# Kernel tuning notes

Hardware: AMD Instinct MI355X
Metric: run time of the kernel (lower is better)

Reference implementation:

```python
import jax, jax.numpy as jnp
import numpy as np

EPS = 1e-08


def setup_inputs() -> dict:
    key = jax.random.key(0)
    k1, k2 = jax.random.split(key)
    query_features = jax.random.normal(k1, (64, 1024, 32, 32), dtype=jnp.float32)
    support_features = jax.random.normal(k2, (25, 1024, 32, 32), dtype=jnp.float32)
    return {"query_features": query_features, "support_features": support_features}


def reference(query_features, support_features):
    B, C, h, w = support_features.shape
    NQ = query_features.shape[0]
    # Covariance over channels: flatten support to (C, B*h*w), center, GEMM.
    support = jnp.transpose(support_features, (1, 0, 2, 3)).reshape(C, -1)
    centered = support - jnp.mean(support, axis=1, keepdims=True)
    N = B * h * w
    cov = (centered @ centered.T) / (N - 1 + EPS)  # (C, C)
    # Queries: (NQ, C, d), L2-normalize each channel row over spatial dim.
    q = query_features.reshape(NQ, C, -1)
    q = q / (jnp.linalg.norm(q, axis=2, keepdims=True) + EPS)
    # diag(q^T cov q) without materializing (d, d): cov@q then elementwise reduce over C.
    cq = jnp.einsum('cD,nDd->ncd', cov, q)  # (NQ, C, d)
    scores = jnp.mean(jnp.sum(q * cq, axis=1), axis=1)  # (NQ,)
    return scores
```

## Files before the change

kernel.cpp:

```cpp
#include <hip/hip_runtime.h>

#define NQ   64
#define CCH  1024
#define DSP  1024
#define NSUP 25600
#define NKT  400

typedef __attribute__((ext_vector_type(4))) float f32x4;
typedef __attribute__((ext_vector_type(8))) __bf16 bf16x8;

#define WAITVM(N) asm volatile("s_waitcnt vmcnt(" #N ")" ::: "memory")
#define WAITLGKM0() asm volatile("s_waitcnt lgkmcnt(0)" ::: "memory")
#define BAR() __builtin_amdgcn_s_barrier()
#define SCHED0() __builtin_amdgcn_sched_barrier(0)

__device__ inline unsigned short f2bf(float x) {
  unsigned u = __builtin_bit_cast(unsigned, x);
  u += 0x7fffu + ((u >> 16) & 1u);
  return (unsigned short)(u >> 16);
}

__global__ __launch_bounds__(256) void zero_kernel(float4* __restrict__ cov4,
                                                   float4* __restrict__ out4) {
  const int i = blockIdx.x * 256 + threadIdx.x;
  cov4[i] = make_float4(0.f, 0.f, 0.f, 0.f);
  if (i < 16) out4[i] = make_float4(0.f, 0.f, 0.f, 0.f);
}


__global__ __launch_bounds__(512) void mean_center_kernel(
    const float* __restrict__ sup, float* __restrict__ mean,
    unsigned short* __restrict__ Sb, int write_sb) {
  __shared__ float4 row[6400];
  __shared__ float red[512];
  const int c = blockIdx.x;
  const int tid = threadIdx.x;
  float s = 0.f;
  for (int qd = tid; qd < 6400; qd += 512) {
    const int b = qd >> 8, s4 = (qd & 255) << 2;
    const float4 v = *(const float4*)(sup + ((size_t)b * CCH + c) * DSP + s4);
    row[qd] = v;
    s += v.x + v.y + v.z + v.w;
  }
  red[tid] = s;
  __syncthreads();
  for (int st = 256; st > 0; st >>= 1) {
    if (tid < st) red[tid] += red[tid + st];
    __syncthreads();
  }
  const float m = red[0] * (1.0f / 25600.0f);
  if (tid == 0) mean[c] = m;
  if (write_sb) {
    for (int qd = tid; qd < 6400; qd += 512) {
      const float4 v = row[qd];
      const int b = qd >> 8, s4 = (qd & 255) << 2;
      ushort4 o;
      o.x = f2bf(v.x - m); o.y = f2bf(v.y - m);
      o.z = f2bf(v.z - m); o.w = f2bf(v.w - m);
      *(ushort4*)(Sb + (size_t)c * NSUP + b * DSP + s4) = o;
    }
  }
}

__global__ __launch_bounds__(256) void qnorm_kernel(
    const float* __restrict__ q, float* __restrict__ qfac,
    unsigned short* __restrict__ Qb, int write_qb) {
  const int row = blockIdx.x * 4 + (threadIdx.x >> 6);
  const int l = threadIdx.x & 63;
  const float4* src = (const float4*)(q + (size_t)row * DSP);
  float4 v[4];
  float ss = 0.f;
#pragma unroll
  for (int i = 0; i < 4; ++i) {
    v[i] = src[l + 64 * i];
    ss += v[i].x * v[i].x + v[i].y * v[i].y + v[i].z * v[i].z + v[i].w * v[i].w;
  }
#pragma unroll
  for (int off = 32; off > 0; off >>= 1) ss += __shfl_xor(ss, off);
  const float f = 1.0f / (sqrtf(ss) + 1e-8f);
  if (l == 0) qfac[row] = f;
  if (write_qb) {
#pragma unroll
    for (int i = 0; i < 4; ++i) {
      ushort4 o;
      o.x = f2bf(v[i].x * f); o.y = f2bf(v[i].y * f);
      o.z = f2bf(v[i].z * f); o.w = f2bf(v[i].w * f);
      *(ushort4*)(Qb + (size_t)row * DSP + (size_t)(l + 64 * i) * 4) = o;
    }
  }
}


__device__ inline void rd4(const unsigned short* base, int r0, int col, int lr, bf16x8 f[4]) {
#pragma unroll
  for (int i = 0; i < 4; ++i)
    f[i] = *(const bf16x8*)(const void*)(base + (r0 + i * 16 + lr) * 64 + col);
}
__device__ inline void mfma16(const bf16x8 a[4], const bf16x8 b[4], f32x4 (*acc)[4]) {
  __builtin_amdgcn_s_setprio(1);
#pragma unroll
  for (int i = 0; i < 4; ++i)
#pragma unroll
    for (int j = 0; j < 4; ++j)
      acc[i][j] = __builtin_amdgcn_mfma_f32_16x16x32_bf16(a[i], b[j], acc[i][j], 0, 0, 0);
  __builtin_amdgcn_s_setprio(0);
}

__device__ inline void stage_glds(const unsigned short* __restrict__ src, int ld,
                                  int row0, int k0, unsigned short* lds) {
  const int tid = threadIdx.x;
  const int w = tid >> 6;
#pragma unroll
  for (int it = 0; it < 4; ++it) {
    const int ci = it * 256 + tid;
    const int r = ci >> 3;
    const int kc = ((ci & 7) ^ (r & 7)) << 3;
    const unsigned short* g = src + (size_t)(row0 + r) * ld + k0 + kc;
    unsigned short* lb = lds + ((it * 256 + w * 64) << 3);
    __builtin_amdgcn_global_load_lds((const __attribute__((address_space(1))) void*)g,
                                     (__attribute__((address_space(3))) void*)lb,
                                     16, 0, 0);
  }
}

__device__ inline void stage256g(const unsigned short* __restrict__ src, int ld,
                                 int row0, int k0, unsigned short* lds_base) {
  const int tid = threadIdx.x;
  const int wid = tid >> 6;
#pragma unroll
  for (int it = 0; it < 4; ++it) {
    const int ci = it * 512 + tid;
    const int r = ci >> 3;
    const int kc = ((ci & 7) ^ (r & 7)) << 3;
    const unsigned short* g = src + (size_t)(row0 + r) * ld + k0 + kc;
    unsigned short* lb = lds_base + ((it * 512 + (wid << 6)) << 3);
    __builtin_amdgcn_global_load_lds((const __attribute__((address_space(1))) void*)g,
                                     (__attribute__((address_space(3))) void*)lb,
                                     16, 0, 0);
  }
}

template <int NT>
__device__ inline void loop256(const unsigned short* __restrict__ src, int ld,
                               int rowA, int rowB, int k0, bool diag,
                               unsigned short* lds,
                               int wm, int wn, int lr, int kg, int sw,
                               f32x4 (*acc)[4]) {
  stage256g(src, ld, rowA, k0, lds);
  if (!diag) stage256g(src, ld, rowB, k0, lds + 16384);
  stage256g(src, ld, rowA, k0 + 64, lds + 32768);
  if (!diag) stage256g(src, ld, rowB, k0 + 64, lds + 32768 + 16384);

  for (int t = 0; t < NT; ++t) {
    const int cb = (t & 1) << 15;
    if (t < NT - 1) { if (diag) { WAITVM(4); } else { WAITVM(8); } }
    else { WAITVM(0); }
    BAR(); SCHED0();
    const unsigned short* A = lds + cb + wm * 8192;
    const unsigned short* B = lds + cb + (diag ? 0 : 16384) + (wn >> 1) * 8192;
    const int brow = (wn & 1) * 64;
    bf16x8 a[4], b[4];
    {
      const int col = kg ^ sw;
      rd4(B, brow, col, lr, b);
      rd4(A, 0, col, lr, a);
      mfma16(a, b, &acc[0]);
      rd4(A, 64, col, lr, a);
      mfma16(a, b, &acc[4]);
    }
    {
      const int col = (32 + kg) ^ sw;
      rd4(B, brow, col, lr, b);
      rd4(A, 0, col, lr, a);
      mfma16(a, b, &acc[0]);
      rd4(A, 64, col, lr, a);
      WAITLGKM0();
      BAR(); SCHED0();
      if (t + 2 < NT) {
        stage256g(src, ld, rowA, k0 + (t + 2) * 64, lds + cb);
        if (!diag) stage256g(src, ld, rowB, k0 + (t + 2) * 64, lds + cb + 16384);
      }
      mfma16(a, b, &acc[4]);
    }
  }
}

__device__ inline void decode_tile8(int t, int& ti, int& tj) {
  int rem = t; ti = 0;
  while (rem >= 8 - ti) { rem -= 8 - ti; ++ti; }
  tj = ti + rem;
}
__device__ inline void decode_pair4(int p, int& ti, int& tj) {
  int rem = p; ti = 0;
  while (rem >= 4 - ti) { rem -= 4 - ti; ++ti; }
  tj = ti + rem;
}

__global__ __launch_bounds__(256) void cov128_kernel(
    const unsigned short* __restrict__ Sb, float* __restrict__ cov) {
  __shared__ unsigned short clds[32768];
  const int wg = blockIdx.x;
  const int ks = wg % 7;
  int ti, tj; decode_tile8(wg / 7, ti, tj);
  const bool diag = (ti == tj);
  const int tid = threadIdx.x, l = tid & 63, w = tid >> 6;
  const int wr = (w >> 1) * 64, wc = (w & 1) * 64, lr = l & 15, kg = (l >> 4) * 8;
  const int sw = (lr & 7) << 3;
  f32x4 acc[4][4];
#pragma unroll
  for (int i = 0; i < 4; ++i)
#pragma unroll
    for (int j = 0; j < 4; ++j) acc[i][j] = 0.f;

  const int kt0 = (NKT * ks) / 7;
  const int nt = (NKT * (ks + 1)) / 7 - kt0;
  const int kbase = kt0 * 64;

  stage_glds(Sb, NSUP, ti * 128, kbase, clds);
  if (!diag) stage_glds(Sb, NSUP, tj * 128, kbase, clds + 8192);
  stage_glds(Sb, NSUP, ti * 128, kbase + 64, clds + 16384);
  if (!diag) stage_glds(Sb, NSUP, tj * 128, kbase + 64, clds + 16384 + 8192);
  for (int t = 0; t < nt; ++t) {
    const int cb = (t & 1) * 16384;
    if (t < nt - 1) { if (diag) { WAITVM(4); } else { WAITVM(8); } }
    else { WAITVM(0); }
    BAR(); SCHED0();
    const unsigned short* A = clds + cb;
    const unsigned short* B = diag ? A : A + 8192;
    const int col0 = kg ^ sw, col1 = (32 + kg) ^ sw;
    bf16x8 a[4], b[4];
    rd4(A, wr, col0, lr, a);
    rd4(B, wc, col0, lr, b);
    mfma16(a, b, (f32x4(*)[4])acc);
    rd4(A, wr, col1, lr, a);
    rd4(B, wc, col1, lr, b);
    WAITLGKM0();
    BAR(); SCHED0();
    if (t + 2 < nt) {
      const int k2 = kbase + (t + 2) * 64;
      stage_glds(Sb, NSUP, ti * 128, k2, clds + cb);
      if (!diag) stage_glds(Sb, NSUP, tj * 128, k2, clds + cb + 8192);
    }
    mfma16(a, b, (f32x4(*)[4])acc);
  }

  const float scale = 1.0f / (25599.0f + 1e-8f);
  const int rbase = ti * 128 + wr + (l >> 4) * 4;
  const int cbase = tj * 128 + wc + (l & 15);
#pragma unroll
  for (int i = 0; i < 4; ++i)
#pragma unroll
    for (int j = 0; j < 4; ++j)
#pragma unroll
      for (int r = 0; r < 4; ++r)
        atomicAdd(&cov[(size_t)(rbase + i * 16 + r) * CCH + cbase + j * 16],
                  acc[i][j][r] * scale);
}

__global__ __launch_bounds__(512, 2) void gram256_kernel(
    const unsigned short* __restrict__ Qb, const float* __restrict__ cov,
    float* __restrict__ out) {
  __shared__ unsigned short lds[65536];
  const int wg = blockIdx.x;
  const int xcd = wg & 7, slot = wg >> 3;
  const int n = xcd * 8 + slot / 10;
  int ti, tj; decode_pair4(slot % 10, ti, tj);
  const bool diag = (ti == tj);
  const int tid = threadIdx.x, l = tid & 63, wid = tid >> 6;
  const int wm = wid >> 2, wn = wid & 3;
  const int lr = l & 15, kg = (l >> 4) * 8;
  const int sw = (lr & 7) << 3;
  const unsigned short* Qn = Qb + (size_t)n * CCH * DSP;

  f32x4 acc[8][4];
#pragma unroll
  for (int i = 0; i < 8; ++i)
#pragma unroll
    for (int j = 0; j < 4; ++j) acc[i][j] = 0.f;

  loop256<16>(Qn, DSP, ti * 256, tj * 256, 0, diag, lds,
              wm, wn, lr, kg, sw, acc);

  float wgt;
  if (!diag) wgt = 2.0f;
  else if (wm == 0 && (wn >> 1) == 1) wgt = 2.0f;
  else if (wm == 1 && (wn >> 1) == 0) wgt = 0.0f;
  else wgt = 1.0f;

  float s = 0.f;
  if (wgt != 0.0f) {
    const int rbase = ti * 256 + wm * 128 + (l >> 4) * 4;
    const int cbase = tj * 256 + wn * 64 + (l & 15);
#pragma unroll
    for (int i = 0; i < 8; ++i)
#pragma unroll
      for (int j = 0; j < 4; ++j)
#pragma unroll
        for (int r = 0; r < 4; ++r)
          s += acc[i][j][r] * cov[(size_t)(rbase + i * 16 + r) * CCH + cbase + j * 16];
  }
  s *= wgt * (1.0f / 1024.0f);
#pragma unroll
  for (int off = 32; off > 0; off >>= 1) s += __shfl_xor(s, off);
  if (l == 0) atomicAdd(&out[n], s);
}

__device__ inline void mfma16s(const bf16x8 a[4], const bf16x8 b[4], f32x4 acc[4][4]) {
#pragma unroll
  for (int i = 0; i < 4; ++i)
#pragma unroll
    for (int j = 0; j < 4; ++j)
      acc[i][j] = __builtin_amdgcn_mfma_f32_16x16x32_bf16(a[i], b[j], acc[i][j], 0, 0, 0);
}

__device__ inline void stage_sup_f32(const float* __restrict__ sup,
                                     const float* __restrict__ mean,
                                     int row0, int k0, unsigned short* lds) {
  const int tid = threadIdx.x;
#pragma unroll
  for (int it = 0; it < 4; ++it) {
    const int ci = it * 256 + tid;
    const int r = ci >> 3, kc = (ci & 7) << 3;
    const int c = row0 + r;
    const int k = k0 + kc;
    const int b = k >> 10, sp = k & 1023;
    const float4* gp = (const float4*)(sup + ((size_t)b * CCH + c) * DSP + sp);
    const float4 v0 = gp[0], v1 = gp[1];
    const float m = mean[c];
    union { unsigned short h[8]; int4 q; } pk;
    pk.h[0] = f2bf(v0.x - m); pk.h[1] = f2bf(v0.y - m);
    pk.h[2] = f2bf(v0.z - m); pk.h[3] = f2bf(v0.w - m);
    pk.h[4] = f2bf(v1.x - m); pk.h[5] = f2bf(v1.y - m);
    pk.h[6] = f2bf(v1.z - m); pk.h[7] = f2bf(v1.w - m);
    *(int4*)(lds + (size_t)(r * 8 + ((ci & 7) ^ (r & 7))) * 8) = pk.q;
  }
}
__device__ inline void stage_q_f32(const float* __restrict__ qn,
                                   const float* __restrict__ qfacn,
                                   int row0, int k0, unsigned short* lds) {
  const int tid = threadIdx.x;
#pragma unroll
  for (int it = 0; it < 4; ++it) {
    const int ci = it * 256 + tid;
    const int r = ci >> 3, kc = (ci & 7) << 3;
    const int c = row0 + r;
    const float4* gp = (const float4*)(qn + (size_t)c * DSP + k0 + kc);
    const float4 v0 = gp[0], v1 = gp[1];
    const float f = qfacn[c];
    union { unsigned short h[8]; int4 q; } pk;
    pk.h[0] = f2bf(v0.x * f); pk.h[1] = f2bf(v0.y * f);
    pk.h[2] = f2bf(v0.z * f); pk.h[3] = f2bf(v0.w * f);
    pk.h[4] = f2bf(v1.x * f); pk.h[5] = f2bf(v1.y * f);
    pk.h[6] = f2bf(v1.z * f); pk.h[7] = f2bf(v1.w * f);
    *(int4*)(lds + (size_t)(r * 8 + ((ci & 7) ^ (r & 7))) * 8) = pk.q;
  }
}
__device__ inline void compute_step(const unsigned short* lA, const unsigned short* lB,
                                    int wr, int wc, int lr, int kg, f32x4 acc[4][4]) {
  const int sc = (lr & 7) << 3;
#pragma unroll
  for (int kk = 0; kk < 64; kk += 32) {
    const int col = (kk + kg) ^ sc;
    bf16x8 a[4], b[4];
    rd4(lA, wr, col, lr, a);
    rd4(lB, wc, col, lr, b);
    mfma16s(a, b, acc);
  }
}

__global__ __launch_bounds__(256) void cov_kernel_f32(
    const float* __restrict__ sup, const float* __restrict__ mean,
    float* __restrict__ cov) {
  __shared__ unsigned short clds[32768];
  const int wg = blockIdx.x;
  const int ks = wg & 7;
  int ti, tj; decode_tile8(wg >> 3, ti, tj);
  const bool diag = (ti == tj);
  const int tid = threadIdx.x, l = tid & 63, w = tid >> 6;
  const int wr = (w >> 1) * 64, wc = (w & 1) * 64, lr = l & 15, kg = (l >> 4) * 8;
  f32x4 acc[4][4];
#pragma unroll
  for (int i = 0; i < 4; ++i)
#pragma unroll
    for (int j = 0; j < 4; ++j) acc[i][j] = 0.f;

  const int kbase = ks * (NSUP / 8);
  stage_sup_f32(sup, mean, ti * 128, kbase, clds);
  if (!diag) stage_sup_f32(sup, mean, tj * 128, kbase, clds + 8192);
  __syncthreads();
  for (int kt = 0; kt < 50; ++kt) {
    const int cb = (kt & 1) * 16384;
    const int nb = cb ^ 16384;
    if (kt + 1 < 50) {
      const int k1 = kbase + (kt + 1) * 64;
      stage_sup_f32(sup, mean, ti * 128, k1, clds + nb);
      if (!diag) stage_sup_f32(sup, mean, tj * 128, k1, clds + nb + 8192);
    }
    compute_step(clds + cb, diag ? clds + cb : clds + cb + 8192, wr, wc, lr, kg, acc);
    __syncthreads();
  }
  const float scale = 1.0f / (25599.0f + 1e-8f);
  const int rbase = ti * 128 + wr + (l >> 4) * 4;
  const int cbase = tj * 128 + wc + (l & 15);
#pragma unroll
  for (int i = 0; i < 4; ++i)
#pragma unroll
    for (int j = 0; j < 4; ++j)
#pragma unroll
      for (int r = 0; r < 4; ++r)
        atomicAdd(&cov[(size_t)(rbase + i * 16 + r) * CCH + cbase + j * 16],
                  acc[i][j][r] * scale);
}

__global__ __launch_bounds__(256) void gram_kernel_f32(
    const float* __restrict__ q, const float* __restrict__ qfac,
    const float* __restrict__ cov, float* __restrict__ out) {
  __shared__ unsigned short lA[2][128 * 64];
  __shared__ unsigned short lB[2][128 * 64];
  const int wg = blockIdx.x;
  const int xcd = wg & 7, slot = wg >> 3;
  const int n = xcd * 8 + slot / 36;
  int ti, tj; decode_tile8(slot % 36, ti, tj);
  const bool diag = (ti == tj);
  const int tid = threadIdx.x, l = tid & 63, w = tid >> 6;
  const int wr = (w >> 1) * 64, wc = (w & 1) * 64, lr = l & 15, kg = (l >> 4) * 8;
  f32x4 acc[4][4];
#pragma unroll
  for (int i = 0; i < 4; ++i)
#pragma unroll
    for (int j = 0; j < 4; ++j) acc[i][j] = 0.f;

  const float* qn = q + (size_t)n * CCH * DSP;
  const float* qfacn = qfac + (size_t)n * CCH;

  stage_q_f32(qn, qfacn, ti * 128, 0, lA[0]);
  if (!diag) stage_q_f32(qn, qfacn, tj * 128, 0, lB[0]);
  __syncthreads();
  int cur = 0;
  for (int kt = 0; kt < 16; ++kt) {
    if (kt + 1 < 16) {
      const int k1 = (kt + 1) * 64;
      stage_q_f32(qn, qfacn, ti * 128, k1, lA[cur ^ 1]);
      if (!diag) stage_q_f32(qn, qfacn, tj * 128, k1, lB[cur ^ 1]);
    }
    compute_step(lA[cur], diag ? lA[cur] : lB[cur], wr, wc, lr, kg, acc);
    __syncthreads();
    cur ^= 1;
  }

  float s = 0.f;
  const int rbase = ti * 128 + wr + (l >> 4) * 4;
  const int cbase = tj * 128 + wc + (l & 15);
#pragma unroll
  for (int i = 0; i < 4; ++i)
#pragma unroll
    for (int j = 0; j < 4; ++j)
#pragma unroll
      for (int r = 0; r < 4; ++r)
        s += acc[i][j][r] * cov[(size_t)(rbase + i * 16 + r) * CCH + cbase + j * 16];
  if (!diag) s *= 2.0f;
  s *= (1.0f / 1024.0f);
#pragma unroll
  for (int off = 32; off > 0; off >>= 1) s += __shfl_xor(s, off);
  if (l == 0) atomicAdd(&out[n], s);
}

extern "C" void kernel_launch(void* const* d_in, const int* in_sizes, int n_in,
                              void* d_out, int out_size, void* d_ws, size_t ws_size,
                              hipStream_t stream) {
  const float* q = (const float*)d_in[0];
  const float* sup = (const float*)d_in[1];
  float* out = (float*)d_out;

  char* ws = (char*)d_ws;
  float* mean = (float*)ws;
  float* qfac = (float*)(ws + (4 << 10));
  float* cov  = (float*)(ws + (4 << 10) + (256 << 10));
  unsigned short* Sb = (unsigned short*)(ws + (4 << 10) + (256 << 10) + (4 << 20));
  unsigned short* Qb = Sb + (size_t)CCH * NSUP;
  const size_t need_fat = (size_t)(4 << 10) + (256 << 10) + (4 << 20) +
                          (size_t)CCH * NSUP * 2 + (size_t)NQ * CCH * DSP * 2;
  const bool fat = ws_size >= need_fat;

  zero_kernel<<<1024, 256, 0, stream>>>((float4*)cov, (float4*)out);

  mean_center_kernel<<<CCH, 512, 0, stream>>>(sup, mean, Sb, fat ? 1 : 0);
  qnorm_kernel<<<NQ * CCH / 4, 256, 0, stream>>>(q, qfac, Qb, fat ? 1 : 0);

  if (fat) {
    cov128_kernel<<<dim3(252), 256, 0, stream>>>(Sb, cov);
    gram256_kernel<<<dim3(640), 512, 0, stream>>>(Qb, cov, out);
  } else {
    cov_kernel_f32<<<dim3(288), 256, 0, stream>>>(sup, mean, cov);
    gram_kernel_f32<<<dim3(8 * 8 * 36), 256, 0, stream>>>(q, qfac, cov, out);
  }
}
```

Before: 271.5 us.

## Fuse covariance and gram kernels into one persistent launch with atomic ticket ordering

Merges the cov128 and gram256 kernels into a single 640-block launch. Blocks take a ticket from an atomic counter, and the first 252 tickets first compute a covariance split-K tile (now 512 threads, with the k-halves split across waves) and then signal a completion counter. Every block then computes its query gram tile and spin-waits on that counter only before its final cov-weighted reduction. This overlaps the gram MFMA work with the covariance phase and removes a kernel boundary. In exchange it adds spin-wait and atomic traffic, and the cov blocks occupy 512-thread slots with a different wave split.

```diff
diff --git a/kernel.cpp b/kernel.cpp
--- a/kernel.cpp
+++ b/kernel.cpp
@@ -5,6 +5,7 @@
 #define DSP  1024
 #define NSUP 25600
 #define NKT  400
+#define NCOV 252
 
 typedef __attribute__((ext_vector_type(4))) float f32x4;
 typedef __attribute__((ext_vector_type(8))) __bf16 bf16x8;
@@ -21,10 +22,12 @@
 }
 
 __global__ __launch_bounds__(256) void zero_kernel(float4* __restrict__ cov4,
-                                                   float4* __restrict__ out4) {
+                                                   float4* __restrict__ out4,
+                                                   int* __restrict__ ctrs) {
   const int i = blockIdx.x * 256 + threadIdx.x;
   cov4[i] = make_float4(0.f, 0.f, 0.f, 0.f);
   if (i < 16) out4[i] = make_float4(0.f, 0.f, 0.f, 0.f);
+  if (blockIdx.x == 0 && threadIdx.x < 64) ctrs[threadIdx.x] = 0;
 }
 
 
@@ -106,17 +109,17 @@
   __builtin_amdgcn_s_setprio(0);
 }
 
-__device__ inline void stage_glds(const unsigned short* __restrict__ src, int ld,
-                                  int row0, int k0, unsigned short* lds) {
+__device__ inline void stage128_512(const unsigned short* __restrict__ src, int ld,
+                                    int row0, int k0, unsigned short* lds) {
   const int tid = threadIdx.x;
   const int w = tid >> 6;
 #pragma unroll
-  for (int it = 0; it < 4; ++it) {
-    const int ci = it * 256 + tid;
+  for (int it = 0; it < 2; ++it) {
+    const int ci = it * 512 + tid;
     const int r = ci >> 3;
     const int kc = ((ci & 7) ^ (r & 7)) << 3;
     const unsigned short* g = src + (size_t)(row0 + r) * ld + k0 + kc;
-    unsigned short* lb = lds + ((it * 256 + w * 64) << 3);
+    unsigned short* lb = lds + ((it * 512 + (w << 6)) << 3);
     __builtin_amdgcn_global_load_lds((const __attribute__((address_space(1))) void*)g,
                                      (__attribute__((address_space(3))) void*)lb,
                                      16, 0, 0);
@@ -140,20 +143,108 @@
   }
 }
 
-template <int NT>
-__device__ inline void loop256(const unsigned short* __restrict__ src, int ld,
-                               int rowA, int rowB, int k0, bool diag,
-                               unsigned short* lds,
-                               int wm, int wn, int lr, int kg, int sw,
-                               f32x4 (*acc)[4]) {
-  stage256g(src, ld, rowA, k0, lds);
-  if (!diag) stage256g(src, ld, rowB, k0, lds + 16384);
-  stage256g(src, ld, rowA, k0 + 64, lds + 32768);
-  if (!diag) stage256g(src, ld, rowB, k0 + 64, lds + 32768 + 16384);
-
-  for (int t = 0; t < NT; ++t) {
-    const int cb = (t & 1) << 15;
-    if (t < NT - 1) { if (diag) { WAITVM(4); } else { WAITVM(8); } }
+__device__ inline void decode_tile8(int t, int& ti, int& tj) {
+  int rem = t; ti = 0;
+  while (rem >= 8 - ti) { rem -= 8 - ti; ++ti; }
+  tj = ti + rem;
+}
+__device__ inline void decode_pair4(int p, int& ti, int& tj) {
+  int rem = p; ti = 0;
+  while (rem >= 4 - ti) { rem -= 4 - ti; ++ti; }
+  tj = ti + rem;
+}
+
+__global__ __launch_bounds__(512, 2) void fused_kernel(
+    const unsigned short* __restrict__ Sb, const unsigned short* __restrict__ Qb,
+    float* __restrict__ cov, int* __restrict__ ctrs, float* __restrict__ out) {
+  __shared__ unsigned short lds[65536];
+  __shared__ int tick_s;
+  const int tid = threadIdx.x, l = tid & 63, wid = tid >> 6;
+  if (tid == 0) tick_s = atomicAdd(&ctrs[0], 1);
+  __syncthreads();
+  const int t = tick_s;
+  const int lr = l & 15, kg = (l >> 4) * 8;
+  const int sw = (lr & 7) << 3;
+
+  if (t < NCOV) {
+    const int ks = t % 7;
+    int ci_, cj_; decode_tile8(t / 7, ci_, cj_);
+    const bool cdiag = (ci_ == cj_);
+    const int quad = wid & 3, kh = wid >> 2;
+    const int wr = (quad >> 1) * 64, wc = (quad & 1) * 64;
+    const int kt0 = (NKT * ks) / 7;
+    const int nt = (NKT * (ks + 1)) / 7 - kt0;
+    const int kbase = kt0 * 64;
+    f32x4 acc4[4][4];
+#pragma unroll
+    for (int i = 0; i < 4; ++i)
+#pragma unroll
+      for (int j = 0; j < 4; ++j) acc4[i][j] = 0.f;
+
+    stage128_512(Sb, NSUP, ci_ * 128, kbase, lds);
+    if (!cdiag) stage128_512(Sb, NSUP, cj_ * 128, kbase, lds + 8192);
+    stage128_512(Sb, NSUP, ci_ * 128, kbase + 64, lds + 16384);
+    if (!cdiag) stage128_512(Sb, NSUP, cj_ * 128, kbase + 64, lds + 16384 + 8192);
+    for (int k = 0; k < nt; ++k) {
+      const int cb = (k & 1) * 16384;
+      if (k < nt - 1) { if (cdiag) { WAITVM(2); } else { WAITVM(4); } }
+      else { WAITVM(0); }
+      BAR(); SCHED0();
+      const unsigned short* A = lds + cb;
+      const unsigned short* B = cdiag ? A : A + 8192;
+      const int col = (kh * 32 + kg) ^ sw;
+      bf16x8 a[4], b[4];
+      rd4(A, wr, col, lr, a);
+      rd4(B, wc, col, lr, b);
+      WAITLGKM0();
+      BAR(); SCHED0();
+      if (k + 2 < nt) {
+        const int k2 = kbase + (k + 2) * 64;
+        stage128_512(Sb, NSUP, ci_ * 128, k2, lds + cb);
+        if (!cdiag) stage128_512(Sb, NSUP, cj_ * 128, k2, lds + cb + 8192);
+      }
+      mfma16(a, b, acc4);
+    }
+    const float scale = 1.0f / (25599.0f + 1e-8f);
+    const int rbase = ci_ * 128 + wr + (l >> 4) * 4;
+    const int cbase = cj_ * 128 + wc + (l & 15);
+#pragma unroll
+    for (int i = 0; i < 4; ++i)
+#pragma unroll
+      for (int j = 0; j < 4; ++j)
+#pragma unroll
+        for (int r = 0; r < 4; ++r)
+          atomicAdd(&cov[(size_t)(rbase + i * 16 + r) * CCH + cbase + j * 16],
+                    acc4[i][j][r] * scale);
+    __threadfence();
+    __syncthreads();
+    if (tid == 0)
+      __hip_atomic_fetch_add(&ctrs[1], 1, __ATOMIC_RELEASE, __HIP_MEMORY_SCOPE_AGENT);
+    __syncthreads();
+  }
+
+  const int xcd = t & 7, slot = t >> 3;
+  const int n = xcd * 8 + slot / 10;
+  int ti, tj; decode_pair4(slot % 10, ti, tj);
+  const bool diag = (ti == tj);
+  const int wm = wid >> 2, wn = wid & 3;
+  const unsigned short* Qn = Qb + (size_t)n * CCH * DSP;
+  const int rowA = ti * 256, rowB = tj * 256;
+
+  f32x4 acc[8][4];
+#pragma unroll
+  for (int i = 0; i < 8; ++i)
+#pragma unroll
+    for (int j = 0; j < 4; ++j) acc[i][j] = 0.f;
+
+  stage256g(Qn, DSP, rowA, 0, lds);
+  if (!diag) stage256g(Qn, DSP, rowB, 0, lds + 16384);
+  stage256g(Qn, DSP, rowA, 64, lds + 32768);
+  if (!diag) stage256g(Qn, DSP, rowB, 64, lds + 32768 + 16384);
+
+  for (int k = 0; k < 16; ++k) {
+    const int cb = (k & 1) << 15;
+    if (k < 15) { if (diag) { WAITVM(4); } else { WAITVM(8); } }
     else { WAITVM(0); }
     BAR(); SCHED0();
     const unsigned short* A = lds + cb + wm * 8192;
@@ -176,110 +267,19 @@
       rd4(A, 64, col, lr, a);
       WAITLGKM0();
       BAR(); SCHED0();
-      if (t + 2 < NT) {
-        stage256g(src, ld, rowA, k0 + (t + 2) * 64, lds + cb);
-        if (!diag) stage256g(src, ld, rowB, k0 + (t + 2) * 64, lds + cb + 16384);
+      if (k + 2 < 16) {
+        stage256g(Qn, DSP, rowA, (k + 2) * 64, lds + cb);
+        if (!diag) stage256g(Qn, DSP, rowB, (k + 2) * 64, lds + cb + 16384);
       }
       mfma16(a, b, &acc[4]);
     }
   }
-}
-
-__device__ inline void decode_tile8(int t, int& ti, int& tj) {
-  int rem = t; ti = 0;
-  while (rem >= 8 - ti) { rem -= 8 - ti; ++ti; }
-  tj = ti + rem;
-}
-__device__ inline void decode_pair4(int p, int& ti, int& tj) {
-  int rem = p; ti = 0;
-  while (rem >= 4 - ti) { rem -= 4 - ti; ++ti; }
-  tj = ti + rem;
-}
-
-__global__ __launch_bounds__(256) void cov128_kernel(
-    const unsigned short* __restrict__ Sb, float* __restrict__ cov) {
-  __shared__ unsigned short clds[32768];
-  const int wg = blockIdx.x;
-  const int ks = wg % 7;
-  int ti, tj; decode_tile8(wg / 7, ti, tj);
-  const bool diag = (ti == tj);
-  const int tid = threadIdx.x, l = tid & 63, w = tid >> 6;
-  const int wr = (w >> 1) * 64, wc = (w & 1) * 64, lr = l & 15, kg = (l >> 4) * 8;
-  const int sw = (lr & 7) << 3;
-  f32x4 acc[4][4];
-#pragma unroll
-  for (int i = 0; i < 4; ++i)
-#pragma unroll
-    for (int j = 0; j < 4; ++j) acc[i][j] = 0.f;
-
-  const int kt0 = (NKT * ks) / 7;
-  const int nt = (NKT * (ks + 1)) / 7 - kt0;
-  const int kbase = kt0 * 64;
-
-  stage_glds(Sb, NSUP, ti * 128, kbase, clds);
-  if (!diag) stage_glds(Sb, NSUP, tj * 128, kbase, clds + 8192);
-  stage_glds(Sb, NSUP, ti * 128, kbase + 64, clds + 16384);
-  if (!diag) stage_glds(Sb, NSUP, tj * 128, kbase + 64, clds + 16384 + 8192);
-  for (int t = 0; t < nt; ++t) {
-    const int cb = (t & 1) * 16384;
-    if (t < nt - 1) { if (diag) { WAITVM(4); } else { WAITVM(8); } }
-    else { WAITVM(0); }
-    BAR(); SCHED0();
-    const unsigned short* A = clds + cb;
-    const unsigned short* B = diag ? A : A + 8192;
-    const int col0 = kg ^ sw, col1 = (32 + kg) ^ sw;
-    bf16x8 a[4], b[4];
-    rd4(A, wr, col0, lr, a);
-    rd4(B, wc, col0, lr, b);
-    mfma16(a, b, (f32x4(*)[4])acc);
-    rd4(A, wr, col1, lr, a);
-    rd4(B, wc, col1, lr, b);
-    WAITLGKM0();
-    BAR(); SCHED0();
-    if (t + 2 < nt) {
-      const int k2 = kbase + (t + 2) * 64;
-      stage_glds(Sb, NSUP, ti * 128, k2, clds + cb);
-      if (!diag) stage_glds(Sb, NSUP, tj * 128, k2, clds + cb + 8192);
-    }
-    mfma16(a, b, (f32x4(*)[4])acc);
-  }
-
-  const float scale = 1.0f / (25599.0f + 1e-8f);
-  const int rbase = ti * 128 + wr + (l >> 4) * 4;
-  const int cbase = tj * 128 + wc + (l & 15);
-#pragma unroll
-  for (int i = 0; i < 4; ++i)
-#pragma unroll
-    for (int j = 0; j < 4; ++j)
-#pragma unroll
-      for (int r = 0; r < 4; ++r)
-        atomicAdd(&cov[(size_t)(rbase + i * 16 + r) * CCH + cbase + j * 16],
-                  acc[i][j][r] * scale);
-}
-
-__global__ __launch_bounds__(512, 2) void gram256_kernel(
-    const unsigned short* __restrict__ Qb, const float* __restrict__ cov,
-    float* __restrict__ out) {
-  __shared__ unsigned short lds[65536];
-  const int wg = blockIdx.x;
-  const int xcd = wg & 7, slot = wg >> 3;
-  const int n = xcd * 8 + slot / 10;
-  int ti, tj; decode_pair4(slot % 10, ti, tj);
-  const bool diag = (ti == tj);
-  const int tid = threadIdx.x, l = tid & 63, wid = tid >> 6;
-  const int wm = wid >> 2, wn = wid & 3;
-  const int lr = l & 15, kg = (l >> 4) * 8;
-  const int sw = (lr & 7) << 3;
-  const unsigned short* Qn = Qb + (size_t)n * CCH * DSP;
-
-  f32x4 acc[8][4];
-#pragma unroll
-  for (int i = 0; i < 8; ++i)
-#pragma unroll
-    for (int j = 0; j < 4; ++j) acc[i][j] = 0.f;
-
-  loop256<16>(Qn, DSP, ti * 256, tj * 256, 0, diag, lds,
-              wm, wn, lr, kg, sw, acc);
+
+  if (tid == 0) {
+    while (__hip_atomic_load(&ctrs[1], __ATOMIC_ACQUIRE, __HIP_MEMORY_SCOPE_AGENT) < NCOV)
+      __builtin_amdgcn_s_sleep(8);
+  }
+  __syncthreads();
 
   float wgt;
   if (!diag) wgt = 2.0f;
@@ -296,8 +296,12 @@
 #pragma unroll
       for (int j = 0; j < 4; ++j)
 #pragma unroll
-        for (int r = 0; r < 4; ++r)
-          s += acc[i][j][r] * cov[(size_t)(rbase + i * 16 + r) * CCH + cbase + j * 16];
+        for (int r = 0; r < 4; ++r) {
+          const float cv = __hip_atomic_load(
+              &cov[(size_t)(rbase + i * 16 + r) * CCH + cbase + j * 16],
+              __ATOMIC_RELAXED, __HIP_MEMORY_SCOPE_AGENT);
+          s += acc[i][j][r] * cv;
+        }
   }
   s *= wgt * (1.0f / 1024.0f);
 #pragma unroll
@@ -476,20 +480,20 @@
   float* mean = (float*)ws;
   float* qfac = (float*)(ws + (4 << 10));
   float* cov  = (float*)(ws + (4 << 10) + (256 << 10));
-  unsigned short* Sb = (unsigned short*)(ws + (4 << 10) + (256 << 10) + (4 << 20));
+  int* ctrs = (int*)(ws + (4 << 10) + (256 << 10) + (4 << 20));
+  unsigned short* Sb = (unsigned short*)(ws + (4 << 10) + (256 << 10) + (4 << 20) + 256);
   unsigned short* Qb = Sb + (size_t)CCH * NSUP;
-  const size_t need_fat = (size_t)(4 << 10) + (256 << 10) + (4 << 20) +
+  const size_t need_fat = (size_t)(4 << 10) + (256 << 10) + (4 << 20) + 256 +
                           (size_t)CCH * NSUP * 2 + (size_t)NQ * CCH * DSP * 2;
   const bool fat = ws_size >= need_fat;
 
-  zero_kernel<<<1024, 256, 0, stream>>>((float4*)cov, (float4*)out);
+  zero_kernel<<<1024, 256, 0, stream>>>((float4*)cov, (float4*)out, ctrs);
 
   mean_center_kernel<<<CCH, 512, 0, stream>>>(sup, mean, Sb, fat ? 1 : 0);
   qnorm_kernel<<<NQ * CCH / 4, 256, 0, stream>>>(q, qfac, Qb, fat ? 1 : 0);
 
   if (fat) {
-    cov128_kernel<<<dim3(252), 256, 0, stream>>>(Sb, cov);
-    gram256_kernel<<<dim3(640), 512, 0, stream>>>(Qb, cov, out);
+    fused_kernel<<<dim3(640), 512, 0, stream>>>(Sb, Qb, cov, ctrs, out);
   } else {
     cov_kernel_f32<<<dim3(288), 256, 0, stream>>>(sup, mean, cov);
     gram_kernel_f32<<<dim3(8 * 8 * 36), 256, 0, stream>>>(q, qfac, cov, out);
```

Result: slower. 332.5 us (+22.5%).
